# Kernel optimization log

Measured on AMD Instinct MI355X. Metric: run time of the kernel, lower is better.

## Reference

```python
import jax, jax.numpy as jnp
import numpy as np

ALPHA = 0.2  # LeakyReLU negative slope
NEG_BIG = -9e15

def setup_inputs() -> dict:
    key = jax.random.key(0)
    k1, k2, k3, k4 = jax.random.split(key, 4)
    B, N, Fin, Fout = 32, 1024, 64, 64
    x = jax.random.normal(k1, (B, N, Fin), dtype=jnp.float32)
    adj = jax.random.randint(k2, (B, N, N), 0, 2, dtype=jnp.int32)
    W = jax.random.normal(k3, (Fin, Fout), dtype=jnp.float32) * (1.414 / np.sqrt(Fin))
    a = jax.random.normal(k4, (2 * Fout, 1), dtype=jnp.float32) * 0.1
    return {"x": x, "adj": adj, "W": W, "a": a}

def reference(x, adj, W, a):
    # x: [B,N,Fin], adj: [B,N,N], W: [Fin,Fout], a: [2*Fout,1]
    h = jnp.einsum('bnf,fo->bno', x, W)               # [B,N,Fout]
    Fout = W.shape[1]
    a1 = a[:Fout, 0]                                   # source half
    a2 = a[Fout:, 0]                                   # target half
    # e_ij = leakyrelu(a1.h_i + a2.h_j)  (equivalent to concat+matmul)
    f = h @ a1                                         # [B,N]
    g = h @ a2                                         # [B,N]
    e = jax.nn.leaky_relu(f[:, :, None] + g[:, None, :], ALPHA)  # [B,N,N]
    att = jnp.where(adj > 0, e, jnp.float32(NEG_BIG))
    att = jax.nn.softmax(att, axis=2)                  # dropout p=0, eval mode
    h_prime = jnp.einsum('bij,bjo->bio', att, h)       # [B,N,Fout]
    return jax.nn.elu(h_prime)                         # concat=True -> elu
```

## Files before the change

### kernel.cpp

```cpp
#include <hip/hip_runtime.h>
#include <hip/hip_bf16.h>
#include <hip/hip_fp16.h>

#define NN 1024
#define FD 64
#define BB 32

typedef __attribute__((ext_vector_type(4))) float    f32x4;
typedef __attribute__((ext_vector_type(8))) _Float16 f16x8;

static __device__ __forceinline__ unsigned short f2hu(float x) {
  _Float16 h = (_Float16)x;
  return __builtin_bit_cast(unsigned short, h);
}
static __device__ __forceinline__ f16x8 bch(int4 v) {
  return __builtin_bit_cast(f16x8, v);
}

__global__ __launch_bounds__(256) void gat_k1(
    const float* __restrict__ x, const float* __restrict__ W,
    const float* __restrict__ av, float* __restrict__ fv,
    float* __restrict__ gv, unsigned short* __restrict__ hF)
{
  __shared__ __align__(16) float Wl[FD * FD];
  __shared__ __align__(16) float xl[FD * 68];
  __shared__ __align__(16) unsigned short tl[FD * 64];
  __shared__ __align__(16) float al[2 * FD];

  const int tid = threadIdx.x;
  const int b   = blockIdx.x >> 4;
  const int n0  = (blockIdx.x & 15) << 6;

  if (tid < 32) ((f32x4*)al)[tid] = ((const f32x4*)av)[tid];
  {
    const int r  = tid >> 2;
    const int cb = (tid & 3) << 2;
    const f32x4* Wg = (const f32x4*)W;
    const f32x4* xg = (const f32x4*)(x + ((size_t)(b * NN + n0)) * FD);
#pragma unroll
    for (int k = 0; k < 4; ++k) {
      f32x4 wv = Wg[r * 16 + cb + k];
      f32x4 xv = xg[r * 16 + cb + k];
      *(f32x4*)(Wl + r * FD + ((cb + k) << 2)) = wv;
      *(f32x4*)(xl + r * 68 + ((cb + k) << 2)) = xv;
    }
  }
  __syncthreads();

  const int r  = tid >> 2;
  const int o0 = (tid & 3) << 4;
  float acc[16];
#pragma unroll
  for (int i = 0; i < 16; ++i) acc[i] = 0.f;

#pragma unroll 8
  for (int f = 0; f < FD; ++f) {
    float xv = xl[r * 68 + f];
    const f32x4* wr = (const f32x4*)(Wl + f * FD + o0);
#pragma unroll
    for (int c = 0; c < 4; ++c) {
      f32x4 wv = wr[c];
      acc[c * 4 + 0] += xv * wv.x;
      acc[c * 4 + 1] += xv * wv.y;
      acc[c * 4 + 2] += xv * wv.z;
      acc[c * 4 + 3] += xv * wv.w;
    }
  }

  float fp = 0.f, gp = 0.f;
#pragma unroll
  for (int i = 0; i < 16; ++i) {
    fp += acc[i] * al[o0 + i];
    gp += acc[i] * al[FD + o0 + i];
  }
  fp += __shfl_xor(fp, 1); fp += __shfl_xor(fp, 2);
  gp += __shfl_xor(gp, 1); gp += __shfl_xor(gp, 2);
  if ((tid & 3) == 0) {
    fv[b * NN + n0 + r] = fp;
    gv[b * NN + n0 + r] = gp;
  }

#pragma unroll
  for (int i = 0; i < 16; ++i) {
    int o = o0 + i;
    tl[o * 64 + ((((r >> 3) ^ (o & 7)) << 3) | (r & 7))] = f2hu(acc[i]);
  }
  __syncthreads();

  {
    const int jt = n0 >> 6;
#pragma unroll
    for (int hh = 0; hh < 2; ++hh) {
      int u = tid + (hh << 8);
      int frag = u >> 6, l = u & 63;
      int o = ((frag >> 1) << 4) + (l & 15);
      int c = ((frag & 1) << 2) + (l >> 4);
      int4 v = *(const int4*)(tl + o * 64 + ((c ^ (o & 7)) << 3));
      *(int4*)(hF + ((((size_t)(b * 16 + jt)) * 8 + frag) * 64 + l) * 8) = v;
    }
  }
}

__global__ __launch_bounds__(256) void gat_k2(
    const int* __restrict__ adj, const float* __restrict__ fv,
    const float* __restrict__ gv, const unsigned short* __restrict__ hF,
    float* __restrict__ out)
{
  __shared__ __align__(16) float gl[NN];
  __shared__ float red[4];

  const int tid  = threadIdx.x;
  const int b    = blockIdx.x >> 4;
  const int i0   = (blockIdx.x & 15) << 6;
  const int lane = tid & 63, w = tid >> 6;
  const int m16  = lane & 15, hi = lane >> 4;
  const int bN   = b * NN;

  f32x4 g4 = *(const f32x4*)(gv + bN + tid * 4);
  *(f32x4*)(gl + tid * 4) = g4;
  float gm = fmaxf(fmaxf(g4.x, g4.y), fmaxf(g4.z, g4.w));
  float fm = fv[bN + i0 + lane];
#pragma unroll
  for (int m = 1; m < 64; m <<= 1) {
    gm = fmaxf(gm, __shfl_xor(gm, m));
    fm = fmaxf(fm, __shfl_xor(fm, m));
  }
  if (lane == 0) red[w] = gm;
  const float fr = fv[bN + i0 + w * 16 + m16];
  __syncthreads();
  gm = fmaxf(fmaxf(red[0], red[1]), fmaxf(red[2], red[3]));
  const float sm = fm + gm;
  const float Cb = fmaxf(sm, 0.2f * sm);

  const int*  adjP = adj + ((size_t)(bN + i0 + w * 16 + m16)) * NN + hi * 8;
  const int4* hFb  = (const int4*)hF + (size_t)b * 8192 + lane;

  float dAcc = 0.f;
  f32x4 acc[4];
#pragma unroll
  for (int n = 0; n < 4; ++n) acc[n] = (f32x4){0.f, 0.f, 0.f, 0.f};

  int4 Aa0, Aa1, Aa2, Aa3, Ba0, Ba1, Ba2, Ba3;

#define LADJ(P, t) do { const int o_ = (t) << 6;        \
    P##0 = *(const int4*)(adjP + o_);                   \
    P##1 = *(const int4*)(adjP + o_ + 4);               \
    P##2 = *(const int4*)(adjP + o_ + 32);              \
    P##3 = *(const int4*)(adjP + o_ + 36); } while (0)

#define PCOMP(dst, ia, ib, ga, gb) do {                                    \
    float e0 = fr + ga.x, e1 = fr + ga.y, e2 = fr + ga.z, e3 = fr + ga.w;  \
    float e4 = fr + gb.x, e5 = fr + gb.y, e6 = fr + gb.z, e7 = fr + gb.w;  \
    e0 = fmaxf(e0, 0.2f * e0) - Cb; e1 = fmaxf(e1, 0.2f * e1) - Cb;        \
    e2 = fmaxf(e2, 0.2f * e2) - Cb; e3 = fmaxf(e3, 0.2f * e3) - Cb;        \
    e4 = fmaxf(e4, 0.2f * e4) - Cb; e5 = fmaxf(e5, 0.2f * e5) - Cb;        \
    e6 = fmaxf(e6, 0.2f * e6) - Cb; e7 = fmaxf(e7, 0.2f * e7) - Cb;        \
    float p0 = (ia.x > 0) ? __expf(e0) : 0.f;                              \
    float p1 = (ia.y > 0) ? __expf(e1) : 0.f;                              \
    float p2 = (ia.z > 0) ? __expf(e2) : 0.f;                              \
    float p3 = (ia.w > 0) ? __expf(e3) : 0.f;                              \
    float p4 = (ib.x > 0) ? __expf(e4) : 0.f;                              \
    float p5 = (ib.y > 0) ? __expf(e5) : 0.f;                              \
    float p6 = (ib.z > 0) ? __expf(e6) : 0.f;                              \
    float p7 = (ib.w > 0) ? __expf(e7) : 0.f;                              \
    dAcc += ((p0 + p1) + (p2 + p3)) + ((p4 + p5) + (p6 + p7));             \
    dst = (f16x8){(_Float16)p0, (_Float16)p1, (_Float16)p2, (_Float16)p3,  \
                  (_Float16)p4, (_Float16)p5, (_Float16)p6, (_Float16)p7}; \
  } while (0)

#define TILE(P, t) do {                                                    \
    const int jb_ = (t) << 6;                                              \
    const int4* hp_ = hFb + (size_t)(t) * 512;                             \
    int4 h0_ = hp_[0],   h1_ = hp_[64],  h2_ = hp_[128], h3_ = hp_[192];   \
    int4 h4_ = hp_[256], h5_ = hp_[320], h6_ = hp_[384], h7_ = hp_[448];   \
    f32x4 ga0_ = *(const f32x4*)(gl + jb_ + hi * 8);                       \
    f32x4 ga1_ = *(const f32x4*)(gl + jb_ + hi * 8 + 4);                   \
    f32x4 gb0_ = *(const f32x4*)(gl + jb_ + 32 + hi * 8);                  \
    f32x4 gb1_ = *(const f32x4*)(gl + jb_ + 32 + hi * 8 + 4);              \
    f16x8 pa_, pb_;                                                        \
    PCOMP(pa_, P##0, P##1, ga0_, ga1_);                                    \
    PCOMP(pb_, P##2, P##3, gb0_, gb1_);                                    \
    acc[0] = __builtin_amdgcn_mfma_f32_16x16x32_f16(pa_, bch(h0_), acc[0], 0, 0, 0); \
    acc[0] = __builtin_amdgcn_mfma_f32_16x16x32_f16(pb_, bch(h1_), acc[0], 0, 0, 0); \
    acc[1] = __builtin_amdgcn_mfma_f32_16x16x32_f16(pa_, bch(h2_), acc[1], 0, 0, 0); \
    acc[1] = __builtin_amdgcn_mfma_f32_16x16x32_f16(pb_, bch(h3_), acc[1], 0, 0, 0); \
    acc[2] = __builtin_amdgcn_mfma_f32_16x16x32_f16(pa_, bch(h4_), acc[2], 0, 0, 0); \
    acc[2] = __builtin_amdgcn_mfma_f32_16x16x32_f16(pb_, bch(h5_), acc[2], 0, 0, 0); \
    acc[3] = __builtin_amdgcn_mfma_f32_16x16x32_f16(pa_, bch(h6_), acc[3], 0, 0, 0); \
    acc[3] = __builtin_amdgcn_mfma_f32_16x16x32_f16(pb_, bch(h7_), acc[3], 0, 0, 0); \
  } while (0)

  LADJ(Aa, 0);
  for (int tt = 0; tt < 8; ++tt) {
    LADJ(Ba, 2 * tt + 1);
    TILE(Aa, 2 * tt);
    if (tt < 7) LADJ(Aa, 2 * tt + 2);
    TILE(Ba, 2 * tt + 1);
  }

  dAcc += __shfl_xor(dAcc, 16);
  dAcc += __shfl_xor(dAcc, 32);

  float* outB = out + ((size_t)(bN + i0 + w * 16)) * FD;
#pragma unroll
  for (int rr = 0; rr < 4; ++rr) {
    const int lr = hi * 4 + rr;
    float d   = __shfl(dAcc, lr);
    float inv = d > 0.f ? 1.f / d : 0.f;
#pragma unroll
    for (int n = 0; n < 4; ++n) {
      float v = acc[n][rr] * inv;
      v = v > 0.f ? v : (__expf(v) - 1.f);
      outB[(size_t)lr * FD + n * 16 + m16] = v;
    }
  }
#undef LADJ
#undef PCOMP
#undef TILE
}

extern "C" void kernel_launch(void* const* d_in, const int* in_sizes, int n_in,
                              void* d_out, int out_size, void* d_ws, size_t ws_size,
                              hipStream_t stream) {
  const float* x   = (const float*)d_in[0];
  const int*   adj = (const int*)d_in[1];
  const float* W   = (const float*)d_in[2];
  const float* a   = (const float*)d_in[3];
  float* out = (float*)d_out;

  unsigned short* hF = (unsigned short*)d_ws;
  float* fv = (float*)((char*)d_ws + (size_t)BB * FD * NN * 2);
  float* gv = fv + (size_t)BB * NN;

  gat_k1<<<dim3(BB * 16), dim3(256), 0, stream>>>(x, W, a, fv, gv, hF);
  gat_k2<<<dim3(BB * 16), dim3(256), 0, stream>>>(adj, fv, gv, hF, out);
}
```

Baseline: 44.30 us.

## Stage adjacency and h tiles through LDS with async triple-buffered loads

The attention kernel now uses 128-thread blocks covering 32 rows each, with twice as many blocks. The adjacency and fp16 h tiles are copied straight into a three-stage LDS ring using global_load_lds, paced by explicit vmcnt waits and barriers. The two waves of a block now share each h tile through LDS instead of each loading it from global memory. This aims to hide memory latency and cut redundant h traffic, at the cost of 48KB+ LDS per block, which may limit occupancy, plus a barrier on every tile.

```diff
diff --git a/kernel.cpp b/kernel.cpp
--- a/kernel.cpp
+++ b/kernel.cpp
@@ -15,6 +15,11 @@
 }
 static __device__ __forceinline__ f16x8 bch(int4 v) {
   return __builtin_bit_cast(f16x8, v);
+}
+static __device__ __forceinline__ void gld16(const void* g, void* l) {
+  __builtin_amdgcn_global_load_lds(
+      (const __attribute__((address_space(1))) void*)g,
+      (__attribute__((address_space(3))) void*)l, 16, 0, 0);
 }
 
 __global__ __launch_bounds__(256) void gat_k1(
@@ -86,7 +91,6 @@
     tl[o * 64 + ((((r >> 3) ^ (o & 7)) << 3) | (r & 7))] = f2hu(acc[i]);
   }
   __syncthreads();
-
   {
     const int jt = n0 >> 6;
 #pragma unroll
@@ -101,60 +105,75 @@
   }
 }
 
-__global__ __launch_bounds__(256) void gat_k2(
+__global__ __launch_bounds__(128) void gat_k2(
     const int* __restrict__ adj, const float* __restrict__ fv,
     const float* __restrict__ gv, const unsigned short* __restrict__ hF,
     float* __restrict__ out)
 {
+  __shared__ __align__(16) char stg[3][16384];
   __shared__ __align__(16) float gl[NN];
-  __shared__ float red[4];
+  __shared__ float red[2];
 
   const int tid  = threadIdx.x;
-  const int b    = blockIdx.x >> 4;
-  const int i0   = (blockIdx.x & 15) << 6;
+  const int b    = blockIdx.x >> 5;
+  const int i0   = (blockIdx.x & 31) << 5;
   const int lane = tid & 63, w = tid >> 6;
   const int m16  = lane & 15, hi = lane >> 4;
   const int bN   = b * NN;
 
-  f32x4 g4 = *(const f32x4*)(gv + bN + tid * 4);
-  *(f32x4*)(gl + tid * 4) = g4;
-  float gm = fmaxf(fmaxf(g4.x, g4.y), fmaxf(g4.z, g4.w));
-  float fm = fv[bN + i0 + lane];
-#pragma unroll
-  for (int m = 1; m < 64; m <<= 1) {
-    gm = fmaxf(gm, __shfl_xor(gm, m));
-    fm = fmaxf(fm, __shfl_xor(fm, m));
-  }
-  if (lane == 0) red[w] = gm;
-  const float fr = fv[bN + i0 + w * 16 + m16];
-  __syncthreads();
-  gm = fmaxf(fmaxf(red[0], red[1]), fmaxf(red[2], red[3]));
-  const float sm = fm + gm;
-  const float Cb = fmaxf(sm, 0.2f * sm);
-
-  const int*  adjP = adj + ((size_t)(bN + i0 + w * 16 + m16)) * NN + hi * 8;
-  const int4* hFb  = (const int4*)hF + (size_t)b * 8192 + lane;
+  {
+    f32x4 ga = ((const f32x4*)(gv + bN))[tid * 2];
+    f32x4 gb = ((const f32x4*)(gv + bN))[tid * 2 + 1];
+    ((f32x4*)gl)[tid * 2]     = ga;
+    ((f32x4*)gl)[tid * 2 + 1] = gb;
+    float gm = fmaxf(fmaxf(fmaxf(ga.x, ga.y), fmaxf(ga.z, ga.w)),
+                     fmaxf(fmaxf(gb.x, gb.y), fmaxf(gb.z, gb.w)));
+    float fm = fv[bN + i0 + (tid & 31)];
+#pragma unroll
+    for (int m = 1; m < 64; m <<= 1) {
+      gm = fmaxf(gm, __shfl_xor(gm, m));
+      fm = fmaxf(fm, __shfl_xor(fm, m));
+    }
+    if (lane == 0) red[w] = gm;
+    const float frt = fv[bN + i0 + w * 16 + m16];
+    __syncthreads();
+    gm = fmaxf(red[0], red[1]);
+    const float sm = fm + gm;
+    const float Cb_ = fmaxf(sm, 0.2f * sm);
+    red[0] = red[0];
+    #define FR frt
+    #define CBV Cb_
+
+  const int*  adjR = adj + ((size_t)(bN + i0 + w * 16 + m16)) * NN + hi * 8;
+  const int4* hFb  = (const int4*)hF + ((size_t)b * 16 * 8) * 64 + lane;
 
   float dAcc = 0.f;
   f32x4 acc[4];
 #pragma unroll
   for (int n = 0; n < 4; ++n) acc[n] = (f32x4){0.f, 0.f, 0.f, 0.f};
 
-  int4 Aa0, Aa1, Aa2, Aa3, Ba0, Ba1, Ba2, Ba3;
-
-#define LADJ(P, t) do { const int o_ = (t) << 6;        \
-    P##0 = *(const int4*)(adjP + o_);                   \
-    P##1 = *(const int4*)(adjP + o_ + 4);               \
-    P##2 = *(const int4*)(adjP + o_ + 32);              \
-    P##3 = *(const int4*)(adjP + o_ + 36); } while (0)
+#define STAGE(jt, p) do {                                                  \
+    const int* ga_ = adjR + (jt) * 64;                                     \
+    char* la_ = stg[p] + w * 4096;                                         \
+    gld16(ga_,      la_);                                                  \
+    gld16(ga_ + 4,  la_ + 1024);                                           \
+    gld16(ga_ + 32, la_ + 2048);                                           \
+    gld16(ga_ + 36, la_ + 3072);                                           \
+    const int4* gh_ = hFb + ((size_t)(jt) * 8 + w * 4) * 64;               \
+    char* lh_ = stg[p] + 8192 + w * 4096;                                  \
+    gld16(gh_,       lh_);                                                 \
+    gld16(gh_ + 64,  lh_ + 1024);                                          \
+    gld16(gh_ + 128, lh_ + 2048);                                          \
+    gld16(gh_ + 192, lh_ + 3072);                                          \
+  } while (0)
 
 #define PCOMP(dst, ia, ib, ga, gb) do {                                    \
-    float e0 = fr + ga.x, e1 = fr + ga.y, e2 = fr + ga.z, e3 = fr + ga.w;  \
-    float e4 = fr + gb.x, e5 = fr + gb.y, e6 = fr + gb.z, e7 = fr + gb.w;  \
-    e0 = fmaxf(e0, 0.2f * e0) - Cb; e1 = fmaxf(e1, 0.2f * e1) - Cb;        \
-    e2 = fmaxf(e2, 0.2f * e2) - Cb; e3 = fmaxf(e3, 0.2f * e3) - Cb;        \
-    e4 = fmaxf(e4, 0.2f * e4) - Cb; e5 = fmaxf(e5, 0.2f * e5) - Cb;        \
-    e6 = fmaxf(e6, 0.2f * e6) - Cb; e7 = fmaxf(e7, 0.2f * e7) - Cb;        \
+    float e0 = FR + ga.x, e1 = FR + ga.y, e2 = FR + ga.z, e3 = FR + ga.w;  \
+    float e4 = FR + gb.x, e5 = FR + gb.y, e6 = FR + gb.z, e7 = FR + gb.w;  \
+    e0 = fmaxf(e0, 0.2f * e0) - CBV; e1 = fmaxf(e1, 0.2f * e1) - CBV;      \
+    e2 = fmaxf(e2, 0.2f * e2) - CBV; e3 = fmaxf(e3, 0.2f * e3) - CBV;      \
+    e4 = fmaxf(e4, 0.2f * e4) - CBV; e5 = fmaxf(e5, 0.2f * e5) - CBV;      \
+    e6 = fmaxf(e6, 0.2f * e6) - CBV; e7 = fmaxf(e7, 0.2f * e7) - CBV;      \
     float p0 = (ia.x > 0) ? __expf(e0) : 0.f;                              \
     float p1 = (ia.y > 0) ? __expf(e1) : 0.f;                              \
     float p2 = (ia.z > 0) ? __expf(e2) : 0.f;                              \
@@ -168,35 +187,51 @@
                   (_Float16)p4, (_Float16)p5, (_Float16)p6, (_Float16)p7}; \
   } while (0)
 
-#define TILE(P, t) do {                                                    \
-    const int jb_ = (t) << 6;                                              \
-    const int4* hp_ = hFb + (size_t)(t) * 512;                             \
-    int4 h0_ = hp_[0],   h1_ = hp_[64],  h2_ = hp_[128], h3_ = hp_[192];   \
-    int4 h4_ = hp_[256], h5_ = hp_[320], h6_ = hp_[384], h7_ = hp_[448];   \
-    f32x4 ga0_ = *(const f32x4*)(gl + jb_ + hi * 8);                       \
-    f32x4 ga1_ = *(const f32x4*)(gl + jb_ + hi * 8 + 4);                   \
-    f32x4 gb0_ = *(const f32x4*)(gl + jb_ + 32 + hi * 8);                  \
-    f32x4 gb1_ = *(const f32x4*)(gl + jb_ + 32 + hi * 8 + 4);              \
-    f16x8 pa_, pb_;                                                        \
-    PCOMP(pa_, P##0, P##1, ga0_, ga1_);                                    \
-    PCOMP(pb_, P##2, P##3, gb0_, gb1_);                                    \
-    acc[0] = __builtin_amdgcn_mfma_f32_16x16x32_f16(pa_, bch(h0_), acc[0], 0, 0, 0); \
-    acc[0] = __builtin_amdgcn_mfma_f32_16x16x32_f16(pb_, bch(h1_), acc[0], 0, 0, 0); \
-    acc[1] = __builtin_amdgcn_mfma_f32_16x16x32_f16(pa_, bch(h2_), acc[1], 0, 0, 0); \
-    acc[1] = __builtin_amdgcn_mfma_f32_16x16x32_f16(pb_, bch(h3_), acc[1], 0, 0, 0); \
-    acc[2] = __builtin_amdgcn_mfma_f32_16x16x32_f16(pa_, bch(h4_), acc[2], 0, 0, 0); \
-    acc[2] = __builtin_amdgcn_mfma_f32_16x16x32_f16(pb_, bch(h5_), acc[2], 0, 0, 0); \
-    acc[3] = __builtin_amdgcn_mfma_f32_16x16x32_f16(pa_, bch(h6_), acc[3], 0, 0, 0); \
-    acc[3] = __builtin_amdgcn_mfma_f32_16x16x32_f16(pb_, bch(h7_), acc[3], 0, 0, 0); \
-  } while (0)
-
-  LADJ(Aa, 0);
-  for (int tt = 0; tt < 8; ++tt) {
-    LADJ(Ba, 2 * tt + 1);
-    TILE(Aa, 2 * tt);
-    if (tt < 7) LADJ(Aa, 2 * tt + 2);
-    TILE(Ba, 2 * tt + 1);
-  }
+  STAGE(0, 0);
+  STAGE(1, 1);
+
+#pragma unroll
+  for (int t = 0; t < 16; ++t) {
+    if (t < 15) { asm volatile("s_waitcnt vmcnt(8)" ::: "memory"); }
+    else        { asm volatile("s_waitcnt vmcnt(0)" ::: "memory"); }
+    __builtin_amdgcn_sched_barrier(0);
+    __builtin_amdgcn_s_barrier();
+    __builtin_amdgcn_sched_barrier(0);
+    const int p = t % 3;
+    const char* sa = stg[p] + w * 4096 + lane * 16;
+    int4 a0 = *(const int4*)(sa);
+    int4 a1 = *(const int4*)(sa + 1024);
+    int4 a2 = *(const int4*)(sa + 2048);
+    int4 a3 = *(const int4*)(sa + 3072);
+    const char* sh = stg[p] + 8192 + lane * 16;
+    int4 h0 = *(const int4*)(sh);
+    int4 h1 = *(const int4*)(sh + 1024);
+    int4 h2 = *(const int4*)(sh + 2048);
+    int4 h3 = *(const int4*)(sh + 3072);
+    int4 h4 = *(const int4*)(sh + 4096);
+    int4 h5 = *(const int4*)(sh + 5120);
+    int4 h6 = *(const int4*)(sh + 6144);
+    int4 h7 = *(const int4*)(sh + 7168);
+    const float* gp_ = gl + t * 64 + hi * 8;
+    f32x4 ga0 = *(const f32x4*)(gp_);
+    f32x4 ga1 = *(const f32x4*)(gp_ + 4);
+    f32x4 gb0 = *(const f32x4*)(gp_ + 32);
+    f32x4 gb1 = *(const f32x4*)(gp_ + 36);
+    f16x8 pa, pb;
+    PCOMP(pa, a0, a1, ga0, ga1);
+    PCOMP(pb, a2, a3, gb0, gb1);
+    acc[0] = __builtin_amdgcn_mfma_f32_16x16x32_f16(pa, bch(h0), acc[0], 0, 0, 0);
+    acc[0] = __builtin_amdgcn_mfma_f32_16x16x32_f16(pb, bch(h1), acc[0], 0, 0, 0);
+    acc[1] = __builtin_amdgcn_mfma_f32_16x16x32_f16(pa, bch(h2), acc[1], 0, 0, 0);
+    acc[1] = __builtin_amdgcn_mfma_f32_16x16x32_f16(pb, bch(h3), acc[1], 0, 0, 0);
+    acc[2] = __builtin_amdgcn_mfma_f32_16x16x32_f16(pa, bch(h4), acc[2], 0, 0, 0);
+    acc[2] = __builtin_amdgcn_mfma_f32_16x16x32_f16(pb, bch(h5), acc[2], 0, 0, 0);
+    acc[3] = __builtin_amdgcn_mfma_f32_16x16x32_f16(pa, bch(h6), acc[3], 0, 0, 0);
+    acc[3] = __builtin_amdgcn_mfma_f32_16x16x32_f16(pb, bch(h7), acc[3], 0, 0, 0);
+    if (t < 14) STAGE(t + 2, (t + 2) % 3);
+  }
+#undef STAGE
+#undef PCOMP
 
   dAcc += __shfl_xor(dAcc, 16);
   dAcc += __shfl_xor(dAcc, 32);
@@ -214,9 +249,9 @@
       outB[(size_t)lr * FD + n * 16 + m16] = v;
     }
   }
-#undef LADJ
-#undef PCOMP
-#undef TILE
+#undef FR
+#undef CBV
+  }
 }
 
 extern "C" void kernel_launch(void* const* d_in, const int* in_sizes, int n_in,
@@ -233,5 +268,5 @@
   float* gv = fv + (size_t)BB * NN;
 
   gat_k1<<<dim3(BB * 16), dim3(256), 0, stream>>>(x, W, a, fv, gv, hF);
-  gat_k2<<<dim3(BB * 16), dim3(256), 0, stream>>>(adj, fv, gv, hF, out);
-}
+  gat_k2<<<dim3(BB * 32), dim3(128), 0, stream>>>(adj, fv, gv, hF, out);
+}
```

New measurement: 150.3 us. 3.39x slower.
